# Performance work log

Measured on AMD Instinct MI355X. Metric: run time of the kernel, lower is better.

## Reference

```python
import jax, jax.numpy as jnp
import numpy as np

WINDOW_SIZE = 11
SIGMA = 1.5
DATA_RANGE = 1.0
CHANNEL = 3
K1 = 0.01
K2 = 0.03
EPS = 1e-08


def _gaussian_window(window_size, sigma, channel):
    # 1D gaussian normalized to sum 1, then outer product -> 2D window
    xs = np.arange(window_size) - window_size // 2
    g = np.exp(-(xs.astype(np.float32) ** 2) / (2.0 * sigma ** 2))
    g = g / g.sum()
    w2d = np.outer(g, g).astype(np.float32)  # [K, K]
    # depthwise kernel in OIHW layout: [channel, 1, K, K]
    return jnp.asarray(np.broadcast_to(w2d, (channel, 1, window_size, window_size)))


def _depthwise_blur(img, window):
    # img: [B, C, H, W], window: [C, 1, K, K]; SAME padding depthwise conv
    pad = WINDOW_SIZE // 2
    return jax.lax.conv_general_dilated(
        img, window,
        window_strides=(1, 1),
        padding=[(pad, pad), (pad, pad)],
        dimension_numbers=("NCHW", "OIHW", "NCHW"),
        feature_group_count=CHANNEL,
    )


def setup_inputs() -> dict:
    key = jax.random.key(0)
    kx, ky = jax.random.split(key)
    x = jax.random.uniform(kx, (32, 3, 512, 512), dtype=jnp.float32)
    y = jax.random.uniform(ky, (32, 3, 512, 512), dtype=jnp.float32)
    return {"x": x, "y": y}


def reference(x, y):
    window = _gaussian_window(WINDOW_SIZE, SIGMA, CHANNEL)
    C1 = (K1 * DATA_RANGE) ** 2
    C2 = (K2 * DATA_RANGE) ** 2

    mu_x = _depthwise_blur(x, window)
    mu_y = _depthwise_blur(y, window)
    mu_x2 = mu_x * mu_x
    mu_y2 = mu_y * mu_y
    mu_xy = mu_x * mu_y

    sigma_x2 = _depthwise_blur(x * x, window) - mu_x2
    sigma_y2 = _depthwise_blur(y * y, window) - mu_y2
    sigma_xy = _depthwise_blur(x * y, window) - mu_xy

    num = (2.0 * mu_xy + C1) * (2.0 * sigma_xy + C2)
    den = (mu_x2 + mu_y2 + C1) * (sigma_x2 + sigma_y2 + C2)
    ssim_map = num / (den + EPS)
    return 1.0 - jnp.mean(ssim_map)
```

## Files before the change

kernel.cpp:

```cpp
#include <hip/hip_runtime.h>

typedef float v4f   __attribute__((ext_vector_type(4)));
typedef float f32x4 __attribute__((ext_vector_type(4)));
typedef _Float16 h4 __attribute__((ext_vector_type(4)));
typedef _Float16 h8 __attribute__((ext_vector_type(8)));

#define HH 512
#define WW 512
#define NPLANES 96
#define NSTRIP 32
#define NHALF 2
#define NBLK (NPLANES * NSTRIP * NHALF)
#define C1V 1e-4f
#define C2V 9e-4f
#define EPSV 1e-8f
#define NPIX 25165824.0f

#define SLOT_B 784
#define Q_B    3136
#define LDS_B  15680

#define MF(A, B) __builtin_amdgcn_mfma_f32_16x16x32_f16((A), (B), zf, 0, 0, 0)

#define SELW(DST, IX) { const int ix_ = (IX); float r_ = 0.f; \
  r_ = (ix_ == 0) ? wv0 : r_;  r_ = (ix_ == 1) ? wv1 : r_; \
  r_ = (ix_ == 2) ? wv2 : r_;  r_ = (ix_ == 3) ? wv3 : r_; \
  r_ = (ix_ == 4) ? wv4 : r_;  r_ = (ix_ == 5) ? wv5 : r_; \
  r_ = (ix_ == 6) ? wv6 : r_;  r_ = (ix_ == 7) ? wv7 : r_; \
  r_ = (ix_ == 8) ? wv8 : r_;  r_ = (ix_ == 9) ? wv9 : r_; \
  r_ = (ix_ == 10) ? wv10 : r_; DST = r_; }

#define PACK8(DST, F0,F1,F2,F3,F4,F5,F6,F7) \
  DST = (h8){(_Float16)(F0),(_Float16)(F1),(_Float16)(F2),(_Float16)(F3), \
             (_Float16)(F4),(_Float16)(F5),(_Float16)(F6),(_Float16)(F7)};

#define EPX(M) { \
  const float mux_ = mx[M], muy_ = my[M]; \
  const float mx2_ = mux_ * mux_, my2_ = muy_ * muy_, mxy_ = mux_ * muy_; \
  const float sx2_ = vx2[M] - mx2_, sy2_ = vy2[M] - my2_, sxy_ = vxy[M] - mxy_; \
  const float num_ = fmaf(2.f, mxy_, C1V) * fmaf(2.f, sxy_, C2V); \
  const float den_ = (mx2_ + my2_ + C1V) * (sx2_ + sy2_ + C2V) + EPSV; \
  acc = fmaf(num_, __builtin_amdgcn_rcpf(den_), acc); }

#define VLOADL(O) { \
  const int c_ = (O) + ((s + 1) >> 1); \
  const char* rb_ = lds + (c_ & 3) * SLOT_B + rByte; \
  vbx  = *(const h8*)(rb_); \
  vby  = *(const h8*)(rb_ + Q_B); \
  vbx2 = *(const h8*)(rb_ + 2 * Q_B); \
  vby2 = *(const h8*)(rb_ + 3 * Q_B); \
  vbxy = *(const h8*)(rb_ + 4 * Q_B); }

#define VMFMA { \
  const f32x4 mx  = MF(Wf, vbx);  const f32x4 my  = MF(Wf, vby); \
  const f32x4 vx2 = MF(Wf, vbx2); const f32x4 vy2 = MF(Wf, vby2); \
  const f32x4 vxy = MF(Wf, vbxy); \
  EPX(0) EPX(1) EPX(2) EPX(3) }

#define STEP(T, CXA,CXB,CYA,CYB) { \
  const int t_ = (T); \
  if (t_ >= 3) VLOADL(t_ - 3) \
  h8 ax, ay; \
  PACK8(ax, CXA[0],CXA[1],CXA[2],CXA[3], CXB[0],CXB[1],CXB[2],CXB[3]) \
  PACK8(ay, CYA[0],CYA[1],CYA[2],CYA[3], CYB[0],CYB[1],CYB[2],CYB[3]) \
  if (t_ + 2 < 18) { \
    const int rb2_ = min(max((Gbase + t_ + 2) * 16, 0), 496); \
    const float* qx_ = xp + (size_t)rb2_ * WW; \
    const float* qy_ = yp + (size_t)rb2_ * WW; \
    CXA = *(const v4f*)(qx_ + offA); CXB = *(const v4f*)(qx_ + offB); \
    CYA = *(const v4f*)(qy_ + offA); CYB = *(const v4f*)(qy_ + offB); \
  } \
  const bool rOK_ = (unsigned)(Gbase + t_) < 32u; \
  const h8 wfh_ = rOK_ ? WfH : (h8)(_Float16)0.f; \
  const h8 ax2 = ax * ax, ay2 = ay * ay, axy = ax * ay; \
  const f32x4 chx  = MF(ax,  wfh_); const f32x4 chy  = MF(ay,  wfh_); \
  const f32x4 chx2 = MF(ax2, wfh_); const f32x4 chy2 = MF(ay2, wfh_); \
  const f32x4 chxy = MF(axy, wfh_); \
  { char* wb_ = lds + (t_ & 3) * SLOT_B + wByte; \
    *(h4*)(wb_)         = (h4){(_Float16)chx[0], (_Float16)chx[1], (_Float16)chx[2], (_Float16)chx[3]}; \
    *(h4*)(wb_ + Q_B)   = (h4){(_Float16)chy[0], (_Float16)chy[1], (_Float16)chy[2], (_Float16)chy[3]}; \
    *(h4*)(wb_ + 2*Q_B) = (h4){(_Float16)chx2[0],(_Float16)chx2[1],(_Float16)chx2[2],(_Float16)chx2[3]}; \
    *(h4*)(wb_ + 3*Q_B) = (h4){(_Float16)chy2[0],(_Float16)chy2[1],(_Float16)chy2[2],(_Float16)chy2[3]}; \
    *(h4*)(wb_ + 4*Q_B) = (h4){(_Float16)chxy[0],(_Float16)chxy[1],(_Float16)chxy[2],(_Float16)chxy[3]}; } \
  if (t_ >= 3) VMFMA }

__global__ __launch_bounds__(64)
void ssim_main(const float* __restrict__ x, const float* __restrict__ y,
               float* __restrict__ partial)
{
  __shared__ __attribute__((aligned(16))) char lds[LDS_B];

  const int l = threadIdx.x;
  const int n = l & 15;
  const int s = l >> 4;

  const int wg = blockIdx.x;
  const int swz = (wg & 7) * (NBLK / 8) + (wg >> 3);
  const int plane = swz >> 6;
  const int rem = swz & 63;
  const int strip = rem & 31;
  const int half = rem >> 5;
  const int C0 = strip * 16;
  const int Gbase = 16 * half - 1;

  const float* xp = x + (size_t)plane * (HH * WW);
  const float* yp = y + (size_t)plane * (HH * WW);

  float wv0, wv1, wv2, wv3, wv4, wv5, wv6, wv7, wv8, wv9, wv10;
#define WINIT(k) wv##k = expf(-((float)((k - 5) * (k - 5))) / 4.5f);
  WINIT(0) WINIT(1) WINIT(2) WINIT(3) WINIT(4) WINIT(5)
  WINIT(6) WINIT(7) WINIT(8) WINIT(9) WINIT(10)
#undef WINIT
  const float inv_ = 1.f / (wv0 + wv1 + wv2 + wv3 + wv4 + wv5 + wv6 + wv7 + wv8 + wv9 + wv10);
#define WNORM(k) wv##k = __int_as_float(__builtin_amdgcn_readfirstlane(__float_as_int(wv##k * inv_)));
  WNORM(0) WNORM(1) WNORM(2) WNORM(3) WNORM(4) WNORM(5)
  WNORM(6) WNORM(7) WNORM(8) WNORM(9) WNORM(10)
#undef WNORM

  const f32x4 zf = {0.f, 0.f, 0.f, 0.f};

  h8 Wf;
  {
    const int kb = 8 * s;
    float b0,b1,b2,b3,b4,b5,b6,b7;
    SELW(b0, kb + 0 - n - 3) SELW(b1, kb + 1 - n - 3)
    SELW(b2, kb + 2 - n - 3) SELW(b3, kb + 3 - n - 3)
    SELW(b4, kb + 4 - n - 3) SELW(b5, kb + 5 - n - 3)
    SELW(b6, kb + 6 - n - 3) SELW(b7, kb + 7 - n - 3)
    PACK8(Wf, b0,b1,b2,b3,b4,b5,b6,b7)
  }

  const int cb = C0 - 8 + 8 * s;
  const bool kill = (cb < 0) || (cb >= WW);
  h8 WfH = Wf;
  if (kill) WfH = (h8)(_Float16)0.f;
  const int ca = kill ? 0 : cb;

  const int offA = n * WW + ca;
  const int offB = offA + 4;

  const int wByte = n * 48 + 8 * s;
  const int rByte = n * 48 + 16 * ((s + 1) & 1);

  h8 vbx, vby, vbx2, vby2, vbxy;
  float acc = 0.f;

  v4f XA0, XB0, YA0, YB0, XA1, XB1, YA1, YB1;
  {
    const int rb0 = min(max(Gbase * 16, 0), 496);
    const int rb1 = min(max((Gbase + 1) * 16, 0), 496);
    const float* q0x = xp + (size_t)rb0 * WW;
    const float* q0y = yp + (size_t)rb0 * WW;
    const float* q1x = xp + (size_t)rb1 * WW;
    const float* q1y = yp + (size_t)rb1 * WW;
    XA0 = *(const v4f*)(q0x + offA); XB0 = *(const v4f*)(q0x + offB);
    YA0 = *(const v4f*)(q0y + offA); YB0 = *(const v4f*)(q0y + offB);
    XA1 = *(const v4f*)(q1x + offA); XB1 = *(const v4f*)(q1x + offB);
    YA1 = *(const v4f*)(q1y + offA); YB1 = *(const v4f*)(q1y + offB);
  }

  #pragma unroll 1
  for (int u = 0; u < 9; ++u) {
    STEP(2 * u,     XA0, XB0, YA0, YB0)
    STEP(2 * u + 1, XA1, XB1, YA1, YB1)
  }
  VLOADL(15) VMFMA

  #pragma unroll
  for (int off = 32; off > 0; off >>= 1) acc += __shfl_down(acc, off);
  if (l == 0) partial[wg] = acc;
}

__global__ void finalize_kernel(const float* __restrict__ partial, float* __restrict__ out)
{
  __shared__ float s4[4];
  float a = 0.f;
  for (int i = threadIdx.x; i < NBLK; i += 256) a += partial[i];
  #pragma unroll
  for (int off = 32; off > 0; off >>= 1) a += __shfl_down(a, off);
  if ((threadIdx.x & 63) == 0) s4[threadIdx.x >> 6] = a;
  __syncthreads();
  if (threadIdx.x == 0) out[0] = 1.f - (s4[0] + s4[1] + s4[2] + s4[3]) * (1.f / NPIX);
}

extern "C" void kernel_launch(void* const* d_in, const int* in_sizes, int n_in,
                              void* d_out, int out_size, void* d_ws, size_t ws_size,
                              hipStream_t stream)
{
  const float* x = (const float*)d_in[0];
  const float* y = (const float*)d_in[1];
  float* ws = (float*)d_ws;
  float* out = (float*)d_out;

  hipLaunchKernelGGL(ssim_main, dim3(NBLK), dim3(64), 0, stream, x, y, ws);
  hipLaunchKernelGGL(finalize_kernel, dim3(1), dim3(256), 0, stream, ws, out);
}
```

Baseline: 69.90 us.

## Process full column strips per wave, two waves per block, split accumulators

Each wave now walks a whole 512-row column strip instead of half of one, which removes the duplicated halo row-block loads and horizontal-pass work at the split between the two halves. Two independent waves are packed into each 128-thread block, each with its own LDS region, and the grid shrinks to a quarter of its former size. The single accumulator becomes four to shorten the dependency chain in the epilogue. In exchange there are fewer blocks in flight and each wave runs a serial loop twice as long, so the tail could be worse balanced.

After: 68.66 us. Within noise of the previous version (-1.8%).

```diff
diff --git a/kernel.cpp b/kernel.cpp
--- a/kernel.cpp
+++ b/kernel.cpp
@@ -9,8 +9,8 @@
 #define WW 512
 #define NPLANES 96
 #define NSTRIP 32
-#define NHALF 2
-#define NBLK (NPLANES * NSTRIP * NHALF)
+#define NUNIT (NPLANES * NSTRIP)
+#define NBLK (NUNIT / 2)
 #define C1V 1e-4f
 #define C2V 9e-4f
 #define EPSV 1e-8f
@@ -18,7 +18,8 @@
 
 #define SLOT_B 784
 #define Q_B    3136
-#define LDS_B  15680
+#define WAVE_B 15680
+#define LDS_B  31360
 
 #define MF(A, B) __builtin_amdgcn_mfma_f32_16x16x32_f16((A), (B), zf, 0, 0, 0)
 
@@ -40,11 +41,11 @@
   const float sx2_ = vx2[M] - mx2_, sy2_ = vy2[M] - my2_, sxy_ = vxy[M] - mxy_; \
   const float num_ = fmaf(2.f, mxy_, C1V) * fmaf(2.f, sxy_, C2V); \
   const float den_ = (mx2_ + my2_ + C1V) * (sx2_ + sy2_ + C2V) + EPSV; \
-  acc = fmaf(num_, __builtin_amdgcn_rcpf(den_), acc); }
+  acc##M = fmaf(num_, __builtin_amdgcn_rcpf(den_), acc##M); }
 
 #define VLOADL(O) { \
-  const int c_ = (O) + ((s + 1) >> 1); \
-  const char* rb_ = lds + (c_ & 3) * SLOT_B + rByte; \
+  const int c_ = (O) - 1 + ((s + 1) >> 1); \
+  const char* rb_ = wlds + (c_ & 3) * SLOT_B + rByte; \
   vbx  = *(const h8*)(rb_); \
   vby  = *(const h8*)(rb_ + Q_B); \
   vbx2 = *(const h8*)(rb_ + 2 * Q_B); \
@@ -57,51 +58,52 @@
   const f32x4 vxy = MF(Wf, vbxy); \
   EPX(0) EPX(1) EPX(2) EPX(3) }
 
-#define STEP(T, CXA,CXB,CYA,CYB) { \
-  const int t_ = (T); \
-  if (t_ >= 3) VLOADL(t_ - 3) \
+#define STEP(TT, CXA,CXB,CYA,CYB) { \
+  const int tt_ = (TT); \
+  if (tt_ >= 3) VLOADL(tt_ - 3) \
   h8 ax, ay; \
   PACK8(ax, CXA[0],CXA[1],CXA[2],CXA[3], CXB[0],CXB[1],CXB[2],CXB[3]) \
   PACK8(ay, CYA[0],CYA[1],CYA[2],CYA[3], CYB[0],CYB[1],CYB[2],CYB[3]) \
-  if (t_ + 2 < 18) { \
-    const int rb2_ = min(max((Gbase + t_ + 2) * 16, 0), 496); \
+  if (tt_ < 32) { \
+    const int rb2_ = min(max(16 * (tt_ + 1), 0), 496); \
     const float* qx_ = xp + (size_t)rb2_ * WW; \
     const float* qy_ = yp + (size_t)rb2_ * WW; \
     CXA = *(const v4f*)(qx_ + offA); CXB = *(const v4f*)(qx_ + offB); \
     CYA = *(const v4f*)(qy_ + offA); CYB = *(const v4f*)(qy_ + offB); \
   } \
-  const bool rOK_ = (unsigned)(Gbase + t_) < 32u; \
+  const bool rOK_ = (unsigned)(tt_ - 1) < 32u; \
   const h8 wfh_ = rOK_ ? WfH : (h8)(_Float16)0.f; \
   const h8 ax2 = ax * ax, ay2 = ay * ay, axy = ax * ay; \
   const f32x4 chx  = MF(ax,  wfh_); const f32x4 chy  = MF(ay,  wfh_); \
   const f32x4 chx2 = MF(ax2, wfh_); const f32x4 chy2 = MF(ay2, wfh_); \
   const f32x4 chxy = MF(axy, wfh_); \
-  { char* wb_ = lds + (t_ & 3) * SLOT_B + wByte; \
+  { char* wb_ = wlds + ((tt_ - 1) & 3) * SLOT_B + wByte; \
     *(h4*)(wb_)         = (h4){(_Float16)chx[0], (_Float16)chx[1], (_Float16)chx[2], (_Float16)chx[3]}; \
     *(h4*)(wb_ + Q_B)   = (h4){(_Float16)chy[0], (_Float16)chy[1], (_Float16)chy[2], (_Float16)chy[3]}; \
     *(h4*)(wb_ + 2*Q_B) = (h4){(_Float16)chx2[0],(_Float16)chx2[1],(_Float16)chx2[2],(_Float16)chx2[3]}; \
     *(h4*)(wb_ + 3*Q_B) = (h4){(_Float16)chy2[0],(_Float16)chy2[1],(_Float16)chy2[2],(_Float16)chy2[3]}; \
     *(h4*)(wb_ + 4*Q_B) = (h4){(_Float16)chxy[0],(_Float16)chxy[1],(_Float16)chxy[2],(_Float16)chxy[3]}; } \
-  if (t_ >= 3) VMFMA }
+  if (tt_ >= 3) VMFMA }
 
-__global__ __launch_bounds__(64)
+__global__ __launch_bounds__(128)
 void ssim_main(const float* __restrict__ x, const float* __restrict__ y,
                float* __restrict__ partial)
 {
   __shared__ __attribute__((aligned(16))) char lds[LDS_B];
 
-  const int l = threadIdx.x;
+  const int l = threadIdx.x & 63;
+  const int wid = threadIdx.x >> 6;
   const int n = l & 15;
   const int s = l >> 4;
 
   const int wg = blockIdx.x;
   const int swz = (wg & 7) * (NBLK / 8) + (wg >> 3);
-  const int plane = swz >> 6;
-  const int rem = swz & 63;
-  const int strip = rem & 31;
-  const int half = rem >> 5;
+  const int unit = swz * 2 + wid;
+  const int plane = unit >> 5;
+  const int strip = unit & 31;
   const int C0 = strip * 16;
-  const int Gbase = 16 * half - 1;
+
+  char* wlds = lds + wid * WAVE_B;
 
   const float* xp = x + (size_t)plane * (HH * WW);
   const float* yp = y + (size_t)plane * (HH * WW);
@@ -143,39 +145,36 @@
   const int rByte = n * 48 + 16 * ((s + 1) & 1);
 
   h8 vbx, vby, vbx2, vby2, vbxy;
-  float acc = 0.f;
+  float acc0 = 0.f, acc1 = 0.f, acc2 = 0.f, acc3 = 0.f;
 
   v4f XA0, XB0, YA0, YB0, XA1, XB1, YA1, YB1;
   {
-    const int rb0 = min(max(Gbase * 16, 0), 496);
-    const int rb1 = min(max((Gbase + 1) * 16, 0), 496);
-    const float* q0x = xp + (size_t)rb0 * WW;
-    const float* q0y = yp + (size_t)rb0 * WW;
-    const float* q1x = xp + (size_t)rb1 * WW;
-    const float* q1y = yp + (size_t)rb1 * WW;
-    XA0 = *(const v4f*)(q0x + offA); XB0 = *(const v4f*)(q0x + offB);
-    YA0 = *(const v4f*)(q0y + offA); YB0 = *(const v4f*)(q0y + offB);
+    const float* q1x = xp;
+    const float* q1y = yp;
+    XA0 = *(const v4f*)(q1x + offA); XB0 = *(const v4f*)(q1x + offB);
+    YA0 = *(const v4f*)(q1y + offA); YB0 = *(const v4f*)(q1y + offB);
     XA1 = *(const v4f*)(q1x + offA); XB1 = *(const v4f*)(q1x + offB);
     YA1 = *(const v4f*)(q1y + offA); YB1 = *(const v4f*)(q1y + offB);
   }
 
   #pragma unroll 1
-  for (int u = 0; u < 9; ++u) {
+  for (int u = 0; u < 17; ++u) {
     STEP(2 * u,     XA0, XB0, YA0, YB0)
     STEP(2 * u + 1, XA1, XB1, YA1, YB1)
   }
-  VLOADL(15) VMFMA
+  VLOADL(31) VMFMA
 
+  float a = (acc0 + acc1) + (acc2 + acc3);
   #pragma unroll
-  for (int off = 32; off > 0; off >>= 1) acc += __shfl_down(acc, off);
-  if (l == 0) partial[wg] = acc;
+  for (int off = 32; off > 0; off >>= 1) a += __shfl_down(a, off);
+  if (l == 0) partial[unit] = a;
 }
 
 __global__ void finalize_kernel(const float* __restrict__ partial, float* __restrict__ out)
 {
   __shared__ float s4[4];
   float a = 0.f;
-  for (int i = threadIdx.x; i < NBLK; i += 256) a += partial[i];
+  for (int i = threadIdx.x; i < NUNIT; i += 256) a += partial[i];
   #pragma unroll
   for (int off = 32; off > 0; off >>= 1) a += __shfl_down(a, off);
   if ((threadIdx.x & 63) == 0) s4[threadIdx.x >> 6] = a;
@@ -192,6 +191,6 @@
   float* ws = (float*)d_ws;
   float* out = (float*)d_out;
 
-  hipLaunchKernelGGL(ssim_main, dim3(NBLK), dim3(64), 0, stream, x, y, ws);
+  hipLaunchKernelGGL(ssim_main, dim3(NBLK), dim3(128), 0, stream, x, y, ws);
   hipLaunchKernelGGL(finalize_kernel, dim3(1), dim3(256), 0, stream, ws, out);
 }
```
